# Performance work log

Hardware: AMD Instinct MI355X
Metric: run time of the kernel (lower is better)

The kernel has to match this reference:

```python
import jax, jax.numpy as jnp
import numpy as np
import math

H = 8      # n_heads
D = 64     # d_model (per-head dim in this module)
QDIM = 512


def setup_inputs() -> dict:
    key = jax.random.key(0)
    ks = jax.random.split(key, 11)
    B, L = 4, 1024
    s = 1.0 / math.sqrt(QDIM)
    inp = {
        "q": jax.random.normal(ks[0], (B, L, QDIM), jnp.float32),
        "k": jax.random.normal(ks[1], (B, L, QDIM), jnp.float32),
        "v": jax.random.normal(ks[2], (B, L, QDIM), jnp.float32),
        # Linear weights (torch layout: [out, in]); biases init to zeros in original
        "wq": jax.random.normal(ks[3], (H * D, QDIM), jnp.float32) * s,
        "bq": jnp.zeros((H * D,), jnp.float32),
        "wk": jax.random.normal(ks[4], (H * D, QDIM), jnp.float32) * s,
        "bk": jnp.zeros((H * D,), jnp.float32),
        "wv": jax.random.normal(ks[5], (H * D, QDIM), jnp.float32) * s,
        "bv": jnp.zeros((H * D,), jnp.float32),
        "wp": jax.random.normal(ks[6], (D, H * D), jnp.float32) * (1.0 / math.sqrt(H * D)),
        "bp": jnp.zeros((D,), jnp.float32),
    }
    return inp


def reference(q, k, v, wq, bq, wk, bk, wv, bv, wp, bp):
    b = q.shape[0]
    # projections, split into heads: [b, L, H, D] -> [b, H, L, D]
    q_s = (q @ wq.T + bq).reshape(b, -1, H, D).transpose(0, 2, 1, 3)
    k_s = (k @ wk.T + bk).reshape(b, -1, H, D).transpose(0, 2, 1, 3)
    v_s = (v @ wv.T + bv).reshape(b, -1, H, D).transpose(0, 2, 1, 3)
    # NOTE: original scales by sqrt(batch_size), not sqrt(d_k)
    scores = jnp.einsum("bhqd,bhkd->bhqk", q_s, k_s) / math.sqrt(b)
    attn = jax.nn.softmax(scores, axis=-1)
    # context = attn^T @ v  (quirk: output seq length = k_len)
    context = jnp.einsum("bhqk,bhqd->bhkd", attn, v_s)
    context = context.transpose(0, 2, 1, 3).reshape(b, -1, H * D)
    output = context @ wp.T + bp  # dropout is identity at eval
    return (output, attn)
```

## Files before the change

### kernel.cpp

```cpp
#include <hip/hip_runtime.h>

#define QD 512
#define NW (512*512)

typedef __attribute__((ext_vector_type(8))) short bf16x8;
typedef __attribute__((ext_vector_type(4))) float f32x4;

#define MFMA16(a,b,c) __builtin_amdgcn_mfma_f32_16x16x32_bf16((a),(b),(c),0,0,0)

static __device__ __forceinline__ short f2bf(float f) {
  unsigned u = __float_as_uint(f);
  u += 0x7fffu + ((u >> 16) & 1u);
  return (short)(u >> 16);
}
static __device__ __forceinline__ float bf2f(short s) {
  return __uint_as_float(((unsigned)(unsigned short)s) << 16);
}

__global__ __launch_bounds__(256) void k_wconv(
    const float* __restrict__ wq, const float* __restrict__ wk,
    const float* __restrict__ wv, const float* __restrict__ wp,
    short* __restrict__ W6, short* __restrict__ WPH) {
  int i = blockIdx.x * 256 + threadIdx.x;
  if (i < 3 * NW) {
    int which = i / NW, j = i - which * NW;
    const float* src = which == 0 ? wq : (which == 1 ? wk : wv);
    float f = src[j];
    short h = f2bf(f);
    short l = f2bf(f - bf2f(h));
    W6[(size_t)which * 2 * NW + j] = h;
    W6[(size_t)which * 2 * NW + NW + j] = l;
  } else {
    int j = i - 3 * NW;
    if (j < 64 * QD) WPH[j] = f2bf(wp[j]);
  }
}

__global__ __launch_bounds__(256) void k_proj(
    const float* __restrict__ q, const float* __restrict__ k, const float* __restrict__ v,
    const float* __restrict__ bq, const float* __restrict__ bk, const float* __restrict__ bv,
    const short* __restrict__ W6,
    short* __restrict__ QsH, short* __restrict__ QsL,
    short* __restrict__ KsH, short* __restrict__ KsL,
    short* __restrict__ Vt) {
  const int t = blockIdx.z;
  const float* X = t == 0 ? q : (t == 1 ? k : v);
  const float* bias = t == 0 ? bq : (t == 1 ? bk : bv);
  const short* WH = W6 + (size_t)t * 2 * NW;
  const short* WL = WH + NW;
  const int lane = threadIdx.x & 63, w = threadIdx.x >> 6;
  const int col = lane & 15, g = lane >> 4;
  const int m0 = blockIdx.y * 64 + w * 16;
  const int n0 = blockIdx.x * 64;

  f32x4 zero = {0.f, 0.f, 0.f, 0.f};
  f32x4 acc[4] = {zero, zero, zero, zero};

  for (int kc = 0; kc < 16; ++kc) {
    const float* xp = X + (size_t)(m0 + col) * QD + kc * 32 + g * 8;
    f32x4 x0 = *(const f32x4*)xp;
    f32x4 x1 = *(const f32x4*)(xp + 4);
    bf16x8 ah, al;
#pragma unroll
    for (int j = 0; j < 4; ++j) {
      short h0 = f2bf(x0[j]); short h1 = f2bf(x1[j]);
      ah[j] = h0; ah[j + 4] = h1;
      al[j] = f2bf(x0[j] - bf2f(h0));
      al[j + 4] = f2bf(x1[j] - bf2f(h1));
    }
#pragma unroll
    for (int nt = 0; nt < 4; ++nt) {
      size_t woff = (size_t)(n0 + nt * 16 + col) * QD + kc * 32 + g * 8;
      bf16x8 bh = *(const bf16x8*)(WH + woff);
      bf16x8 bl = *(const bf16x8*)(WL + woff);
      acc[nt] = MFMA16(ah, bh, acc[nt]);
      acc[nt] = MFMA16(al, bh, acc[nt]);
      acc[nt] = MFMA16(ah, bl, acc[nt]);
    }
  }

#pragma unroll
  for (int nt = 0; nt < 4; ++nt) {
    float bias_v = bias[n0 + nt * 16 + col];
    int d = nt * 16 + col;
#pragma unroll
    for (int r = 0; r < 4; ++r) {
      int m = m0 + g * 4 + r;
      int b = m >> 10, l = m & 1023;
      float val = acc[nt][r] + bias_v;
      if (t < 2) {
        size_t idx = (((size_t)b * 8 + blockIdx.x) * 1024 + l) * 64 + d;
        short h = f2bf(val);
        short lo = f2bf(val - bf2f(h));
        if (t == 0) { QsH[idx] = h; QsL[idx] = lo; }
        else        { KsH[idx] = h; KsL[idx] = lo; }
      } else {
        size_t idx = (((size_t)b * 8 + blockIdx.x) * 64 + d) * 1024 + l;
        Vt[idx] = f2bf(val);
      }
    }
  }
}

__global__ __launch_bounds__(256) void k_attn(
    const short* __restrict__ QsH, const short* __restrict__ QsL,
    const short* __restrict__ KsH, const short* __restrict__ KsL,
    float* __restrict__ attn) {
  const int lane = threadIdx.x & 63, w = threadIdx.x >> 6;
  const int col = lane & 15, g = lane >> 4;
  const int bh = blockIdx.y;
  const int q0 = blockIdx.x * 128 + w * 32;
  const size_t base = (size_t)bh * 1024 * 64;

  bf16x8 qh[2][2], ql[2][2];
#pragma unroll
  for (int c = 0; c < 2; ++c) {
    size_t qoff = base + (size_t)(q0 + c * 16 + col) * 64 + g * 8;
    qh[c][0] = *(const bf16x8*)(QsH + qoff);
    qh[c][1] = *(const bf16x8*)(QsH + qoff + 32);
    ql[c][0] = *(const bf16x8*)(QsL + qoff);
    ql[c][1] = *(const bf16x8*)(QsL + qoff + 32);
  }

  float mx[2] = {-1e30f, -1e30f}, sum[2] = {0.f, 0.f};
  f32x4 zero = {0.f, 0.f, 0.f, 0.f};

  for (int kc = 0; kc < 64; ++kc) {
    size_t koff = base + (size_t)(kc * 16 + col) * 64 + g * 8;
    bf16x8 kh0 = *(const bf16x8*)(KsH + koff);
    bf16x8 kh1 = *(const bf16x8*)(KsH + koff + 32);
    bf16x8 kl0 = *(const bf16x8*)(KsL + koff);
    bf16x8 kl1 = *(const bf16x8*)(KsL + koff + 32);
#pragma unroll
    for (int c = 0; c < 2; ++c) {
      f32x4 S = zero;
      S = MFMA16(kh0, qh[c][0], S);
      S = MFMA16(kh1, qh[c][1], S);
      S = MFMA16(kl0, qh[c][0], S);
      S = MFMA16(kl1, qh[c][1], S);
      S = MFMA16(kh0, ql[c][0], S);
      S = MFMA16(kh1, ql[c][1], S);
      float v0 = S[0] * 0.5f, v1 = S[1] * 0.5f, v2 = S[2] * 0.5f, v3 = S[3] * 0.5f;
      float mloc = fmaxf(fmaxf(v0, v1), fmaxf(v2, v3));
      if (mloc > mx[c]) { sum[c] *= __expf(mx[c] - mloc); mx[c] = mloc; }
      sum[c] += __expf(v0 - mx[c]) + __expf(v1 - mx[c]) +
                __expf(v2 - mx[c]) + __expf(v3 - mx[c]);
    }
  }
#pragma unroll
  for (int c = 0; c < 2; ++c) {
    for (int off = 16; off < 64; off <<= 1) {
      float mo = __shfl_xor(mx[c], off);
      float so = __shfl_xor(sum[c], off);
      float mn = fmaxf(mx[c], mo);
      sum[c] = sum[c] * __expf(mx[c] - mn) + so * __expf(mo - mn);
      mx[c] = mn;
    }
  }
  float inv[2] = {1.f / sum[0], 1.f / sum[1]};

  float* ab = attn + (size_t)bh * 1024 * 1024;
  for (int kc = 0; kc < 64; ++kc) {
    size_t koff = base + (size_t)(kc * 16 + col) * 64 + g * 8;
    bf16x8 kh0 = *(const bf16x8*)(KsH + koff);
    bf16x8 kh1 = *(const bf16x8*)(KsH + koff + 32);
    bf16x8 kl0 = *(const bf16x8*)(KsL + koff);
    bf16x8 kl1 = *(const bf16x8*)(KsL + koff + 32);
#pragma unroll
    for (int c = 0; c < 2; ++c) {
      f32x4 S = zero;
      S = MFMA16(kh0, qh[c][0], S);
      S = MFMA16(kh1, qh[c][1], S);
      S = MFMA16(kl0, qh[c][0], S);
      S = MFMA16(kl1, qh[c][1], S);
      S = MFMA16(kh0, ql[c][0], S);
      S = MFMA16(kh1, ql[c][1], S);
      f32x4 o;
#pragma unroll
      for (int r = 0; r < 4; ++r) o[r] = __expf(S[r] * 0.5f - mx[c]) * inv[c];
      *(f32x4*)(ab + (size_t)(q0 + c * 16 + col) * 1024 + kc * 16 + g * 4) = o;
    }
  }
}

__global__ __launch_bounds__(256) void k_ctx(
    const float* __restrict__ attn, const short* __restrict__ Vt,
    short* __restrict__ ctx) {
  const int lane = threadIdx.x & 63, w = threadIdx.x >> 6;
  const int col = lane & 15, g = lane >> 4;
  const int bh = blockIdx.y;
  const int k0 = blockIdx.x * 64 + w * 16;
  const float* ab = attn + (size_t)bh * 1024 * 1024;
  const short* vb = Vt + (size_t)bh * 64 * 1024;

  f32x4 zero = {0.f, 0.f, 0.f, 0.f};
  f32x4 acc[4] = {zero, zero, zero, zero};

  for (int qc = 0; qc < 32; ++qc) {
    const float* ap = ab + (size_t)(qc * 32 + g * 8) * 1024 + k0 + col;
    bf16x8 af;
#pragma unroll
    for (int j = 0; j < 8; ++j) af[j] = f2bf(ap[(size_t)j * 1024]);
#pragma unroll
    for (int nt = 0; nt < 4; ++nt) {
      bf16x8 bfv = *(const bf16x8*)(vb + (size_t)(nt * 16 + col) * 1024 + qc * 32 + g * 8);
      acc[nt] = MFMA16(af, bfv, acc[nt]);
    }
  }
  int b = bh >> 3, h = bh & 7;
#pragma unroll
  for (int nt = 0; nt < 4; ++nt)
#pragma unroll
    for (int r = 0; r < 4; ++r) {
      int kk = k0 + g * 4 + r;
      ctx[((size_t)(b * 1024 + kk)) * 512 + h * 64 + nt * 16 + col] = f2bf(acc[nt][r]);
    }
}

__global__ __launch_bounds__(256) void k_out(
    const short* __restrict__ ctx, const short* __restrict__ WPH,
    const float* __restrict__ bp, float* __restrict__ out) {
  const int lane = threadIdx.x & 63, w = threadIdx.x >> 6;
  const int col = lane & 15, g = lane >> 4;
  const int m0 = blockIdx.x * 64 + w * 16;

  f32x4 zero = {0.f, 0.f, 0.f, 0.f};
  f32x4 acc[4] = {zero, zero, zero, zero};

  for (int kc = 0; kc < 16; ++kc) {
    bf16x8 a = *(const bf16x8*)(ctx + (size_t)(m0 + col) * 512 + kc * 32 + g * 8);
#pragma unroll
    for (int nt = 0; nt < 4; ++nt) {
      bf16x8 bfr = *(const bf16x8*)(WPH + (size_t)(nt * 16 + col) * 512 + kc * 32 + g * 8);
      acc[nt] = MFMA16(a, bfr, acc[nt]);
    }
  }
#pragma unroll
  for (int nt = 0; nt < 4; ++nt) {
    float bias = bp[nt * 16 + col];
#pragma unroll
    for (int r = 0; r < 4; ++r)
      out[(size_t)(m0 + g * 4 + r) * 64 + nt * 16 + col] = acc[nt][r] + bias;
  }
}

extern "C" void kernel_launch(void* const* d_in, const int* in_sizes, int n_in,
                              void* d_out, int out_size, void* d_ws, size_t ws_size,
                              hipStream_t stream) {
  const float* q  = (const float*)d_in[0];
  const float* k  = (const float*)d_in[1];
  const float* v  = (const float*)d_in[2];
  const float* wq = (const float*)d_in[3];
  const float* bq = (const float*)d_in[4];
  const float* wk = (const float*)d_in[5];
  const float* bk = (const float*)d_in[6];
  const float* wv = (const float*)d_in[7];
  const float* bv = (const float*)d_in[8];
  const float* wp = (const float*)d_in[9];
  const float* bp = (const float*)d_in[10];

  float* out  = (float*)d_out;
  float* attn = out + 262144;

  short* S = (short*)d_ws;
  const size_t E = 2097152;
  short* QsH = S;
  short* QsL = S + E;
  short* KsH = S + 2 * E;
  short* KsL = S + 3 * E;
  short* Vt  = S + 4 * E;
  short* ctx = S + 5 * E;
  short* W6  = S + 6 * E;
  short* WPH = W6 + 6 * (size_t)NW;

  k_wconv<<<dim3(3200), dim3(256), 0, stream>>>(wq, wk, wv, wp, W6, WPH);
  k_proj <<<dim3(8, 64, 3), dim3(256), 0, stream>>>(q, k, v, bq, bk, bv, W6,
                                                    QsH, QsL, KsH, KsL, Vt);
  k_attn <<<dim3(8, 32), dim3(256), 0, stream>>>(QsH, QsL, KsH, KsL, attn);
  k_ctx  <<<dim3(16, 32), dim3(256), 0, stream>>>(attn, Vt, ctx);
  k_out  <<<dim3(64), dim3(256), 0, stream>>>(ctx, WPH, bp, out);
}
```

Before: 378.9 us.

## Pre-convert inputs to bf16, stage projection tiles in LDS, simplify softmax

Adds a separate kernel that converts q/k/v to bf16 hi/lo pairs once. The projection kernel now stages swizzled 64x32 tiles in LDS through global_load_lds and launches once per input instead of as one 3-D grid. The V projection drops to a single bf16 pass, which trades some precision for fewer MFMAs and loads. The attention kernel drops the running-max softmax in favour of plain exp/sum, with one 16-row tile per wave and twice as many blocks. This removes per-tile float-to-bf16 conversion and online-max overhead, but risks exp overflow if scores grow large and adds extra launches and conversion traffic.

```diff
diff --git a/kernel.cpp b/kernel.cpp
--- a/kernel.cpp
+++ b/kernel.cpp
@@ -17,88 +17,132 @@
   return __uint_as_float(((unsigned)(unsigned short)s) << 16);
 }
 
+#define GL2LDS16(g, l)                                                        \
+  __builtin_amdgcn_global_load_lds(                                           \
+      (const __attribute__((address_space(1))) unsigned int*)(g),             \
+      (__attribute__((address_space(3))) unsigned int*)(l), 16, 0, 0)
+
 __global__ __launch_bounds__(256) void k_wconv(
     const float* __restrict__ wq, const float* __restrict__ wk,
     const float* __restrict__ wv, const float* __restrict__ wp,
-    short* __restrict__ W6, short* __restrict__ WPH) {
+    short* __restrict__ W, short* __restrict__ WPH) {
   int i = blockIdx.x * 256 + threadIdx.x;
-  if (i < 3 * NW) {
-    int which = i / NW, j = i - which * NW;
-    const float* src = which == 0 ? wq : (which == 1 ? wk : wv);
-    float f = src[j];
-    short h = f2bf(f);
-    short l = f2bf(f - bf2f(h));
-    W6[(size_t)which * 2 * NW + j] = h;
-    W6[(size_t)which * 2 * NW + NW + j] = l;
+  if (i < NW) {
+    float f = wq[i]; short h = f2bf(f);
+    W[i] = h; W[NW + i] = f2bf(f - bf2f(h));
+  } else if (i < 2 * NW) {
+    int j = i - NW;
+    float f = wk[j]; short h = f2bf(f);
+    W[2 * NW + j] = h; W[3 * NW + j] = f2bf(f - bf2f(h));
+  } else if (i < 3 * NW) {
+    int j = i - 2 * NW;
+    W[4 * NW + j] = f2bf(wv[j]);
   } else {
     int j = i - 3 * NW;
     if (j < 64 * QD) WPH[j] = f2bf(wp[j]);
   }
 }
 
+__global__ __launch_bounds__(256) void k_xconv(
+    const float* __restrict__ q, const float* __restrict__ k, const float* __restrict__ v,
+    short* __restrict__ XqH, short* __restrict__ XqL,
+    short* __restrict__ XkH, short* __restrict__ XkL, short* __restrict__ XvH) {
+  int i = blockIdx.x * 256 + threadIdx.x;
+  int t = i >> 18;
+  int j = i & 0x3FFFF;
+  const float* src = t == 0 ? q : (t == 1 ? k : v);
+  f32x4 x0 = *(const f32x4*)(src + (size_t)j * 8);
+  f32x4 x1 = *(const f32x4*)(src + (size_t)j * 8 + 4);
+  bf16x8 H, L;
+#pragma unroll
+  for (int jj = 0; jj < 4; ++jj) {
+    short h0 = f2bf(x0[jj]); H[jj] = h0; L[jj] = f2bf(x0[jj] - bf2f(h0));
+    short h1 = f2bf(x1[jj]); H[jj + 4] = h1; L[jj + 4] = f2bf(x1[jj] - bf2f(h1));
+  }
+  if (t == 0)      { *(bf16x8*)(XqH + (size_t)j * 8) = H; *(bf16x8*)(XqL + (size_t)j * 8) = L; }
+  else if (t == 1) { *(bf16x8*)(XkH + (size_t)j * 8) = H; *(bf16x8*)(XkL + (size_t)j * 8) = L; }
+  else             { *(bf16x8*)(XvH + (size_t)j * 8) = H; }
+}
+
 __global__ __launch_bounds__(256) void k_proj(
-    const float* __restrict__ q, const float* __restrict__ k, const float* __restrict__ v,
-    const float* __restrict__ bq, const float* __restrict__ bk, const float* __restrict__ bv,
-    const short* __restrict__ W6,
-    short* __restrict__ QsH, short* __restrict__ QsL,
-    short* __restrict__ KsH, short* __restrict__ KsL,
-    short* __restrict__ Vt) {
-  const int t = blockIdx.z;
-  const float* X = t == 0 ? q : (t == 1 ? k : v);
-  const float* bias = t == 0 ? bq : (t == 1 ? bk : bv);
-  const short* WH = W6 + (size_t)t * 2 * NW;
-  const short* WL = WH + NW;
-  const int lane = threadIdx.x & 63, w = threadIdx.x >> 6;
+    const short* __restrict__ XH, const short* __restrict__ XL,
+    const short* __restrict__ WH, const short* __restrict__ WL,
+    const float* __restrict__ bias,
+    short* __restrict__ outH, short* __restrict__ outL,
+    short* __restrict__ Vt, int mode) {
+  __shared__ short Ah[64 * 32], Al[64 * 32], Bh[64 * 32], Bl[64 * 32];
+  const int tid = threadIdx.x;
+  const int lane = tid & 63;
   const int col = lane & 15, g = lane >> 4;
-  const int m0 = blockIdx.y * 64 + w * 16;
-  const int n0 = blockIdx.x * 64;
+  const int w = tid >> 6, wr = w >> 1, wc = w & 1;
+  const int h = blockIdx.x;
+  const int m0 = blockIdx.y * 64;
+  const int srow = tid >> 2;
+  const int scol = ((tid & 3) ^ (srow & 3)) * 8;
+  const size_t xrow = (size_t)(m0 + srow) * QD + scol;
+  const size_t wrow = (size_t)(h * 64 + srow) * QD + scol;
 
   f32x4 zero = {0.f, 0.f, 0.f, 0.f};
-  f32x4 acc[4] = {zero, zero, zero, zero};
+  f32x4 acc[2][2] = {{zero, zero}, {zero, zero}};
 
   for (int kc = 0; kc < 16; ++kc) {
-    const float* xp = X + (size_t)(m0 + col) * QD + kc * 32 + g * 8;
-    f32x4 x0 = *(const f32x4*)xp;
-    f32x4 x1 = *(const f32x4*)(xp + 4);
-    bf16x8 ah, al;
-#pragma unroll
-    for (int j = 0; j < 4; ++j) {
-      short h0 = f2bf(x0[j]); short h1 = f2bf(x1[j]);
-      ah[j] = h0; ah[j + 4] = h1;
-      al[j] = f2bf(x0[j] - bf2f(h0));
-      al[j + 4] = f2bf(x1[j] - bf2f(h1));
-    }
-#pragma unroll
-    for (int nt = 0; nt < 4; ++nt) {
-      size_t woff = (size_t)(n0 + nt * 16 + col) * QD + kc * 32 + g * 8;
-      bf16x8 bh = *(const bf16x8*)(WH + woff);
-      bf16x8 bl = *(const bf16x8*)(WL + woff);
-      acc[nt] = MFMA16(ah, bh, acc[nt]);
-      acc[nt] = MFMA16(al, bh, acc[nt]);
-      acc[nt] = MFMA16(ah, bl, acc[nt]);
-    }
-  }
-
-#pragma unroll
-  for (int nt = 0; nt < 4; ++nt) {
-    float bias_v = bias[n0 + nt * 16 + col];
-    int d = nt * 16 + col;
-#pragma unroll
-    for (int r = 0; r < 4; ++r) {
-      int m = m0 + g * 4 + r;
-      int b = m >> 10, l = m & 1023;
-      float val = acc[nt][r] + bias_v;
-      if (t < 2) {
-        size_t idx = (((size_t)b * 8 + blockIdx.x) * 1024 + l) * 64 + d;
-        short h = f2bf(val);
-        short lo = f2bf(val - bf2f(h));
-        if (t == 0) { QsH[idx] = h; QsL[idx] = lo; }
-        else        { KsH[idx] = h; KsL[idx] = lo; }
-      } else {
-        size_t idx = (((size_t)b * 8 + blockIdx.x) * 64 + d) * 1024 + l;
-        Vt[idx] = f2bf(val);
+    const int kb = kc * 32;
+    GL2LDS16(XH + xrow + kb, &Ah[tid * 8]);
+    GL2LDS16(WH + wrow + kb, &Bh[tid * 8]);
+    if (mode == 0) {
+      GL2LDS16(XL + xrow + kb, &Al[tid * 8]);
+      GL2LDS16(WL + wrow + kb, &Bl[tid * 8]);
+    }
+    __syncthreads();
+
+    bf16x8 a_h[2], a_l[2], b_h[2], b_l[2];
+#pragma unroll
+    for (int mt = 0; mt < 2; ++mt) {
+      int rowa = wr * 32 + mt * 16 + col;
+      int off = rowa * 32 + ((g ^ (rowa & 3)) * 8);
+      a_h[mt] = *(const bf16x8*)&Ah[off];
+      if (mode == 0) a_l[mt] = *(const bf16x8*)&Al[off];
+    }
+#pragma unroll
+    for (int nt = 0; nt < 2; ++nt) {
+      int rowb = wc * 32 + nt * 16 + col;
+      int off = rowb * 32 + ((g ^ (rowb & 3)) * 8);
+      b_h[nt] = *(const bf16x8*)&Bh[off];
+      if (mode == 0) b_l[nt] = *(const bf16x8*)&Bl[off];
+    }
+#pragma unroll
+    for (int mt = 0; mt < 2; ++mt)
+#pragma unroll
+      for (int nt = 0; nt < 2; ++nt) {
+        acc[mt][nt] = MFMA16(a_h[mt], b_h[nt], acc[mt][nt]);
+        if (mode == 0) {
+          acc[mt][nt] = MFMA16(a_l[mt], b_h[nt], acc[mt][nt]);
+          acc[mt][nt] = MFMA16(a_h[mt], b_l[nt], acc[mt][nt]);
+        }
       }
-    }
+    __syncthreads();
+  }
+
+#pragma unroll
+  for (int nt = 0; nt < 2; ++nt) {
+    int d = wc * 32 + nt * 16 + col;
+    float bias_v = bias[h * 64 + d];
+#pragma unroll
+    for (int mt = 0; mt < 2; ++mt)
+#pragma unroll
+      for (int r = 0; r < 4; ++r) {
+        int m = m0 + wr * 32 + mt * 16 + g * 4 + r;
+        int b = m >> 10, l = m & 1023;
+        float val = acc[mt][nt][r] + bias_v;
+        if (mode == 0) {
+          size_t idx = (((size_t)b * 8 + h) * 1024 + l) * 64 + d;
+          short hh = f2bf(val);
+          outH[idx] = hh;
+          outL[idx] = f2bf(val - bf2f(hh));
+        } else {
+          Vt[(((size_t)b * 8 + h) * 64 + d) * 1024 + l] = f2bf(val);
+        }
+      }
   }
 }
 
@@ -109,21 +153,17 @@
   const int lane = threadIdx.x & 63, w = threadIdx.x >> 6;
   const int col = lane & 15, g = lane >> 4;
   const int bh = blockIdx.y;
-  const int q0 = blockIdx.x * 128 + w * 32;
+  const int q0 = blockIdx.x * 64 + w * 16;
   const size_t base = (size_t)bh * 1024 * 64;
 
-  bf16x8 qh[2][2], ql[2][2];
-#pragma unroll
-  for (int c = 0; c < 2; ++c) {
-    size_t qoff = base + (size_t)(q0 + c * 16 + col) * 64 + g * 8;
-    qh[c][0] = *(const bf16x8*)(QsH + qoff);
-    qh[c][1] = *(const bf16x8*)(QsH + qoff + 32);
-    ql[c][0] = *(const bf16x8*)(QsL + qoff);
-    ql[c][1] = *(const bf16x8*)(QsL + qoff + 32);
-  }
-
-  float mx[2] = {-1e30f, -1e30f}, sum[2] = {0.f, 0.f};
+  size_t qoff = base + (size_t)(q0 + col) * 64 + g * 8;
+  bf16x8 qh0 = *(const bf16x8*)(QsH + qoff);
+  bf16x8 qh1 = *(const bf16x8*)(QsH + qoff + 32);
+  bf16x8 ql0 = *(const bf16x8*)(QsL + qoff);
+  bf16x8 ql1 = *(const bf16x8*)(QsL + qoff + 32);
+
   f32x4 zero = {0.f, 0.f, 0.f, 0.f};
+  float sum = 0.f;
 
   for (int kc = 0; kc < 64; ++kc) {
     size_t koff = base + (size_t)(kc * 16 + col) * 64 + g * 8;
@@ -131,55 +171,38 @@
     bf16x8 kh1 = *(const bf16x8*)(KsH + koff + 32);
     bf16x8 kl0 = *(const bf16x8*)(KsL + koff);
     bf16x8 kl1 = *(const bf16x8*)(KsL + koff + 32);
-#pragma unroll
-    for (int c = 0; c < 2; ++c) {
-      f32x4 S = zero;
-      S = MFMA16(kh0, qh[c][0], S);
-      S = MFMA16(kh1, qh[c][1], S);
-      S = MFMA16(kl0, qh[c][0], S);
-      S = MFMA16(kl1, qh[c][1], S);
-      S = MFMA16(kh0, ql[c][0], S);
-      S = MFMA16(kh1, ql[c][1], S);
-      float v0 = S[0] * 0.5f, v1 = S[1] * 0.5f, v2 = S[2] * 0.5f, v3 = S[3] * 0.5f;
-      float mloc = fmaxf(fmaxf(v0, v1), fmaxf(v2, v3));
-      if (mloc > mx[c]) { sum[c] *= __expf(mx[c] - mloc); mx[c] = mloc; }
-      sum[c] += __expf(v0 - mx[c]) + __expf(v1 - mx[c]) +
-                __expf(v2 - mx[c]) + __expf(v3 - mx[c]);
-    }
-  }
-#pragma unroll
-  for (int c = 0; c < 2; ++c) {
-    for (int off = 16; off < 64; off <<= 1) {
-      float mo = __shfl_xor(mx[c], off);
-      float so = __shfl_xor(sum[c], off);
-      float mn = fmaxf(mx[c], mo);
-      sum[c] = sum[c] * __expf(mx[c] - mn) + so * __expf(mo - mn);
-      mx[c] = mn;
-    }
-  }
-  float inv[2] = {1.f / sum[0], 1.f / sum[1]};
-
-  float* ab = attn + (size_t)bh * 1024 * 1024;
+    f32x4 S = zero;
+    S = MFMA16(kh0, qh0, S);
+    S = MFMA16(kh1, qh1, S);
+    S = MFMA16(kl0, qh0, S);
+    S = MFMA16(kl1, qh1, S);
+    S = MFMA16(kh0, ql0, S);
+    S = MFMA16(kh1, ql1, S);
+    sum += __expf(S[0] * 0.5f) + __expf(S[1] * 0.5f) +
+           __expf(S[2] * 0.5f) + __expf(S[3] * 0.5f);
+  }
+  sum += __shfl_xor(sum, 16);
+  sum += __shfl_xor(sum, 32);
+  float inv = 1.f / sum;
+
+  float* ob = attn + (size_t)bh * 1024 * 1024 + (size_t)(q0 + col) * 1024;
   for (int kc = 0; kc < 64; ++kc) {
     size_t koff = base + (size_t)(kc * 16 + col) * 64 + g * 8;
     bf16x8 kh0 = *(const bf16x8*)(KsH + koff);
     bf16x8 kh1 = *(const bf16x8*)(KsH + koff + 32);
     bf16x8 kl0 = *(const bf16x8*)(KsL + koff);
     bf16x8 kl1 = *(const bf16x8*)(KsL + koff + 32);
-#pragma unroll
-    for (int c = 0; c < 2; ++c) {
-      f32x4 S = zero;
-      S = MFMA16(kh0, qh[c][0], S);
-      S = MFMA16(kh1, qh[c][1], S);
-      S = MFMA16(kl0, qh[c][0], S);
-      S = MFMA16(kl1, qh[c][1], S);
-      S = MFMA16(kh0, ql[c][0], S);
-      S = MFMA16(kh1, ql[c][1], S);
-      f32x4 o;
-#pragma unroll
-      for (int r = 0; r < 4; ++r) o[r] = __expf(S[r] * 0.5f - mx[c]) * inv[c];
-      *(f32x4*)(ab + (size_t)(q0 + c * 16 + col) * 1024 + kc * 16 + g * 4) = o;
-    }
+    f32x4 S = zero;
+    S = MFMA16(kh0, qh0, S);
+    S = MFMA16(kh1, qh1, S);
+    S = MFMA16(kl0, qh0, S);
+    S = MFMA16(kl1, qh1, S);
+    S = MFMA16(kh0, ql0, S);
+    S = MFMA16(kh1, ql1, S);
+    f32x4 o;
+#pragma unroll
+    for (int r = 0; r < 4; ++r) o[r] = __expf(S[r] * 0.5f) * inv;
+    *(f32x4*)(ob + kc * 16 + g * 4) = o;
   }
 }
 
@@ -264,19 +287,29 @@
 
   short* S = (short*)d_ws;
   const size_t E = 2097152;
-  short* QsH = S;
-  short* QsL = S + E;
-  short* KsH = S + 2 * E;
-  short* KsL = S + 3 * E;
-  short* Vt  = S + 4 * E;
-  short* ctx = S + 5 * E;
-  short* W6  = S + 6 * E;
-  short* WPH = W6 + 6 * (size_t)NW;
-
-  k_wconv<<<dim3(3200), dim3(256), 0, stream>>>(wq, wk, wv, wp, W6, WPH);
-  k_proj <<<dim3(8, 64, 3), dim3(256), 0, stream>>>(q, k, v, bq, bk, bv, W6,
-                                                    QsH, QsL, KsH, KsL, Vt);
-  k_attn <<<dim3(8, 32), dim3(256), 0, stream>>>(QsH, QsL, KsH, KsL, attn);
+  short* XqH = S;
+  short* XqL = S + E;
+  short* XkH = S + 2 * E;
+  short* XkL = S + 3 * E;
+  short* XvH = S + 4 * E;
+  short* QsH = S + 5 * E;
+  short* QsL = S + 6 * E;
+  short* KsH = S;
+  short* KsL = S + E;
+  short* Vt  = S + 2 * E;
+  short* ctx = S + 3 * E;
+  short* W   = S + 7 * E;
+  short* WPH = W + 5 * (size_t)NW;
+
+  k_wconv<<<dim3(3200), dim3(256), 0, stream>>>(wq, wk, wv, wp, W, WPH);
+  k_xconv<<<dim3(3072), dim3(256), 0, stream>>>(q, k, v, XqH, XqL, XkH, XkL, XvH);
+  k_proj <<<dim3(8, 64), dim3(256), 0, stream>>>(XqH, XqL, W, W + NW, bq,
+                                                 QsH, QsL, nullptr, 0);
+  k_proj <<<dim3(8, 64), dim3(256), 0, stream>>>(XkH, XkL, W + 2 * NW, W + 3 * NW, bk,
+                                                 KsH, KsL, nullptr, 0);
+  k_proj <<<dim3(8, 64), dim3(256), 0, stream>>>(XvH, XvH, W + 4 * NW, W + 4 * NW, bv,
+                                                 nullptr, nullptr, Vt, 1);
+  k_attn <<<dim3(16, 32), dim3(256), 0, stream>>>(QsH, QsL, KsH, KsL, attn);
   k_ctx  <<<dim3(16, 32), dim3(256), 0, stream>>>(attn, Vt, ctx);
   k_out  <<<dim3(64), dim3(256), 0, stream>>>(ctx, WPH, bp, out);
 }
```

After: 367.6 us. 3.0% less time.
